# Kernel tuning notes

Measured on AMD Instinct MI355X. Metric: run time of the kernel, lower is better.

Reference implementation:

```python
import jax, jax.numpy as jnp
import numpy as np

TOP_K = 8  # top_k experts per token


def setup_inputs() -> dict:
    key = jax.random.key(0)
    k1, k2 = jax.random.split(key)
    T, H, E = 16384, 2048, 64
    hidden_states = jax.random.normal(k1, (T, H), dtype=jnp.float32)
    # nn.Linear(hidden_dim, num_experts, bias=False) weight: [E, H]
    gate_w = jax.random.normal(k2, (E, H), dtype=jnp.float32) * (1.0 / np.sqrt(H))
    expert_bias = jnp.zeros((E,), dtype=jnp.float32)  # aux_loss_free bias, init zeros
    return {"hidden_states": hidden_states, "gate_w": gate_w, "expert_bias": expert_bias}


def reference(hidden_states, gate_w, expert_bias):
    # logits: [T, E]
    logits = hidden_states @ gate_w.T
    scores = jax.nn.softmax(logits, axis=-1)  # score_func == 'softmax'
    # aux_loss_free: bias added only for expert selection, not to the probs
    selection_scores = scores + expert_bias[None, :]
    _, topk_indices = jax.lax.top_k(selection_scores, TOP_K)  # [T, K]
    probs = jnp.take_along_axis(scores, topk_indices, axis=-1)  # gather original scores
    probs = probs / (probs.sum(axis=-1, keepdims=True) + 1e-9)  # renormalize (softmax path)
    T, E = scores.shape
    routing_map = jnp.zeros((T, E), dtype=bool).at[jnp.arange(T)[:, None], topk_indices].set(True)
    aux_loss = jnp.zeros((), dtype=scores.dtype)  # load_balance == 'aux_loss_free' -> 0
    return probs, topk_indices, routing_map, aux_loss
```

## Files before the change

kernel.cpp:

```cpp
#include <hip/hip_runtime.h>
#include <math.h>

#define TT 16384
#define HH 2048
#define EE 64
#define KK 8

#define TB 16
#define HC 64
#define NCH (HH / HC)
#define KSPLIT 4
#define CPS (NCH / KSPLIT)
#define TOPC 10
#define MARGIN_REL 8e-5f

#define IDX_OFF ((size_t)TT * KK)
#define MAP_OFF ((size_t)2 * TT * KK)
#define AUX_OFF ((size_t)2 * TT * KK + (size_t)TT * EE)

#define WSPLANE 131072
#define PBUF_B   524288
#define NFLAG_B  17301504
#define LIST_B   17301536
#define RECI_B   17367072
#define RECF_B   18022432
#define NTILE (TT / TB)

typedef short bf16x8 __attribute__((ext_vector_type(8)));
typedef float f32x4  __attribute__((ext_vector_type(4)));

__device__ __forceinline__ unsigned short f2bf(float x) {
    unsigned int u = __float_as_uint(x);
    u += 0x7FFFu + ((u >> 16) & 1u);
    return (unsigned short)(u >> 16);
}
__device__ __forceinline__ float bf2f(unsigned short b) {
    return __uint_as_float(((unsigned int)b) << 16);
}
__device__ __forceinline__ void cvt4(const float4 v, ushort4* hi, ushort4* lo) {
    unsigned short h0 = f2bf(v.x), h1 = f2bf(v.y),
                   h2 = f2bf(v.z), h3 = f2bf(v.w);
    *hi = make_ushort4(h0, h1, h2, h3);
    *lo = make_ushort4(f2bf(v.x - bf2f(h0)), f2bf(v.y - bf2f(h1)),
                       f2bf(v.z - bf2f(h2)), f2bf(v.w - bf2f(h3)));
}

__global__ __launch_bounds__(256)
void prep_kernel(const float* __restrict__ gw, unsigned short* __restrict__ ws,
                 unsigned int* __restrict__ nflag)
{
    if (blockIdx.x == 0 && threadIdx.x == 0) *nflag = 0u;
    const int gid = blockIdx.x * 256 + threadIdx.x;
    const int e  = gid >> 9;
    const int k  = (gid & 511) * 4;
    float4 v = *(const float4*)(gw + (size_t)e * HH + k);
    ushort4 hi, lo;
    cvt4(v, &hi, &lo);
    const int off = (k >> 5) * 2048 + ((k >> 3) & 3) * 512 + e * 8 + (k & 7);
    *(ushort4*)(ws + off)           = hi;
    *(ushort4*)(ws + WSPLANE + off) = lo;
}

#define CHUNKA(C, HV)                                                          \
  do {                                                                         \
    const unsigned short* bp_ = bBase + (size_t)(2 * (C)) * 2048;              \
    bf16x8 Bh0 = *(const bf16x8*)(bp_);                                        \
    bf16x8 Bl0 = *(const bf16x8*)(bp_ + WSPLANE);                              \
    bf16x8 Bh1 = *(const bf16x8*)(bp_ + 2048);                                 \
    bf16x8 Bl1 = *(const bf16x8*)(bp_ + 2048 + WSPLANE);                       \
    unsigned char* buf_ = smem + ((C) & 1) * 4096;                             \
    ushort4 hi_, lo_;                                                          \
    cvt4(HV, &hi_, &lo_);                                                      \
    *(ushort4*)(buf_ + hOff)        = hi_;                                     \
    *(ushort4*)(buf_ + 2048 + hOff) = lo_;                                     \
    __syncthreads();                                                           \
    if ((C) + 2 < climit) HV = *(const float4*)(hgp + ((C) + 2) * HC);         \
    bf16x8 Ah0 = *(const bf16x8*)(buf_ + aOff0);                               \
    bf16x8 Al0 = *(const bf16x8*)(buf_ + 2048 + aOff0);                        \
    bf16x8 Ah1 = *(const bf16x8*)(buf_ + aOff1);                               \
    bf16x8 Al1 = *(const bf16x8*)(buf_ + 2048 + aOff1);                        \
    acc = __builtin_amdgcn_mfma_f32_16x16x32_bf16(Ah0, Bl0, acc, 0, 0, 0);     \
    acc = __builtin_amdgcn_mfma_f32_16x16x32_bf16(Al0, Bh0, acc, 0, 0, 0);     \
    acc = __builtin_amdgcn_mfma_f32_16x16x32_bf16(Ah0, Bh0, acc, 0, 0, 0);     \
    acc = __builtin_amdgcn_mfma_f32_16x16x32_bf16(Ah1, Bl1, acc, 0, 0, 0);     \
    acc = __builtin_amdgcn_mfma_f32_16x16x32_bf16(Al1, Bh1, acc, 0, 0, 0);     \
    acc = __builtin_amdgcn_mfma_f32_16x16x32_bf16(Ah1, Bh1, acc, 0, 0, 0);     \
  } while (0)

__global__ __launch_bounds__(256, 8)
void gemm_partial(const float* __restrict__ hidden,
                  const unsigned short* __restrict__ wsbuf,
                  float* __restrict__ pbuf)
{
    __shared__ __align__(16) unsigned char smem[8192];

    const int tid  = threadIdx.x;
    const int bid  = blockIdx.x;
    const int tile = bid >> 2;
    const int ks   = bid & 3;
    const int tok0 = tile * TB;
    const int c0   = ks * CPS;
    const int climit = c0 + CPS;

    const int hr  = tid >> 4;
    const int hc4 = tid & 15;
    const float* hgp = hidden + (size_t)(tok0 + hr) * HH + hc4 * 4;
    const int hOff = hr * 128 + ((hc4 * 8) ^ ((hr & 7) << 4));

    const int lane = tid & 63;
    const int e0   = (tid >> 6) * 16;
    const int rx   = lane & 15;
    const int kq   = lane >> 4;
    const int aOff0 = rx * 128 + ((kq * 16) ^ ((rx & 7) << 4));
    const int aOff1 = aOff0 ^ 64;
    const unsigned short* bBase = wsbuf + kq * 512 + (e0 + rx) * 8;

    f32x4 acc = {0.f, 0.f, 0.f, 0.f};

    float4 hvA = *(const float4*)(hgp + c0 * HC);
    float4 hvB = *(const float4*)(hgp + (c0 + 1) * HC);

    for (int c = c0; c < climit; c += 2) {
        CHUNKA(c, hvA);
        CHUNKA(c + 1, hvB);
    }

    *(f32x4*)(pbuf + (size_t)bid * 1024 + tid * 4) = acc;
}

__global__ __launch_bounds__(256, 4)
void reduce_epilogue(const float* __restrict__ pbuf,
                     const float* __restrict__ bias,
                     unsigned int* __restrict__ nflag,
                     unsigned int* __restrict__ list,
                     int* __restrict__ recI,
                     float* __restrict__ recF,
                     float* __restrict__ out)
{
    __shared__ __align__(16) float lg[16 * 68 + 8];

    const int tid  = threadIdx.x;
    const int tile = blockIdx.x;
    const int tok0 = tile * TB;

    f32x4 a0 = *(const f32x4*)(pbuf + (size_t)(tile * 4 + 0) * 1024 + tid * 4);
    f32x4 a1 = *(const f32x4*)(pbuf + (size_t)(tile * 4 + 1) * 1024 + tid * 4);
    f32x4 a2 = *(const f32x4*)(pbuf + (size_t)(tile * 4 + 2) * 1024 + tid * 4);
    f32x4 a3 = *(const f32x4*)(pbuf + (size_t)(tile * 4 + 3) * 1024 + tid * 4);
    f32x4 acc = (a0 + a1) + (a2 + a3);

    const int lane = tid & 63;
    const int e0   = (tid >> 6) * 16;
    const int rx   = lane & 15;
    const int kq   = lane >> 4;

    #pragma unroll
    for (int r = 0; r < 4; ++r)
        lg[(4 * kq + r) * 68 + e0 + rx] = acc[r];
    __syncthreads();

    const int t   = tid >> 4;
    const int q   = tid & 15;
    const int tok = tok0 + t;

    float lv[4];
    #pragma unroll
    for (int i = 0; i < 4; ++i) lv[i] = lg[t * 68 + q + 16 * i];

    float mx = lv[0];
    #pragma unroll
    for (int i = 1; i < 4; ++i) mx = fmaxf(mx, lv[i]);
    #pragma unroll
    for (int sh = 1; sh < 16; sh <<= 1) mx = fmaxf(mx, __shfl_xor(mx, sh, 64));

    float ex[4], psum = 0.0f;
    #pragma unroll
    for (int i = 0; i < 4; ++i) { ex[i] = expf(lv[i] - mx); psum += ex[i]; }
    #pragma unroll
    for (int sh = 1; sh < 16; sh <<= 1) psum += __shfl_xor(psum, sh, 64);
    const float inv = 1.0f / psum;

    float pr[4], selv[4];
    #pragma unroll
    for (int i = 0; i < 4; ++i) {
        pr[i]   = ex[i] * inv;
        selv[i] = pr[i] + bias[q + 16 * i];
    }

    float ws_[TOPC], wp[TOPC];
    int   wi[TOPC];
    #pragma unroll
    for (int k = 0; k < TOPC; ++k) {
        float bs = selv[0], bp = pr[0];
        int bi = q;
        #pragma unroll
        for (int i = 1; i < 4; ++i)
            if (selv[i] > bs) { bs = selv[i]; bp = pr[i]; bi = q + 16 * i; }
        #pragma unroll
        for (int sh = 1; sh < 16; sh <<= 1) {
            float os = __shfl_xor(bs, sh, 64);
            float op = __shfl_xor(bp, sh, 64);
            int   ob = __shfl_xor(bi, sh, 64);
            if (os > bs || (os == bs && ob < bi)) { bs = os; bp = op; bi = ob; }
        }
        ws_[k] = bs; wp[k] = bp; wi[k] = bi;
        #pragma unroll
        for (int i = 0; i < 4; ++i)
            if (q + 16 * i == bi) selv[i] = -INFINITY;
    }

    bool flag = false;
    #pragma unroll
    for (int k = 0; k < 8; ++k)
        flag = flag || (ws_[k] - ws_[k + 1] <
                        (ws_[k] + ws_[k + 1]) * MARGIN_REL + 1e-12f);

    {
        int   mywi = wi[0];
        float mywp = wp[0];
        #pragma unroll
        for (int k = 1; k < TOPC; ++k)
            if (q == k) { mywi = wi[k]; mywp = wp[k]; }
        if (flag && q < TOPC) {
            recI[(size_t)tok * 10 + q] = mywi;
            recF[(size_t)tok * 12 + q] = mywp;
        }
        if (flag && q == 0) {
            recF[(size_t)tok * 12 + 10] = mx;
            recF[(size_t)tok * 12 + 11] = inv;
            unsigned int o = atomicAdd(nflag, 1u);
            list[o] = (unsigned int)tok;
        }
    }

    int oi = wi[0];
    float opf = wp[0];
    #pragma unroll
    for (int k = 1; k < 8; ++k)
        if (q == k) { oi = wi[k]; opf = wp[k]; }

    float ps = 0.0f;
    #pragma unroll
    for (int k = 0; k < 8; ++k) ps += wp[k];
    const float rinv = 1.0f / (ps + 1e-9f);

    if (q < KK) {
        out[(size_t)tok * KK + q]           = opf * rinv;
        out[IDX_OFF + (size_t)tok * KK + q] = (float)oi;
    }

    unsigned long long mk = 0ull;
    #pragma unroll
    for (int k = 0; k < 8; ++k) mk |= (1ull << wi[k]);

    {
        float4 a;
        a.x = ((mk >> (4 * q + 0)) & 1ull) ? 1.0f : 0.0f;
        a.y = ((mk >> (4 * q + 1)) & 1ull) ? 1.0f : 0.0f;
        a.z = ((mk >> (4 * q + 2)) & 1ull) ? 1.0f : 0.0f;
        a.w = ((mk >> (4 * q + 3)) & 1ull) ? 1.0f : 0.0f;
        *(float4*)(out + MAP_OFF + (size_t)tok * EE + 4 * q) = a;
    }

    if (tile == 0 && tid == 0) out[AUX_OFF] = 0.0f;
}

__global__ __launch_bounds__(256, 4)
void fixup_kernel(const float* __restrict__ hidden,
                  const float* __restrict__ gate_w,
                  const float* __restrict__ bias,
                  const unsigned int* __restrict__ nflag,
                  const unsigned int* __restrict__ list,
                  const int* __restrict__ recI,
                  const float* __restrict__ recF,
                  float* __restrict__ out)
{
    __shared__ double redL[4][12];

    const int tid  = threadIdx.x;
    const int wv   = tid >> 6;
    const int lane = tid & 63;
    const unsigned int nf = *nflag;

    for (unsigned int i = blockIdx.x; i < nf; i += gridDim.x) {
        const int tok = (int)list[i];

        int   wk[TOPC];
        #pragma unroll
        for (int k = 0; k < TOPC; ++k) wk[k] = recI[(size_t)tok * 10 + k];
        const float mx  = recF[(size_t)tok * 12 + 10];
        const float inv = recF[(size_t)tok * 12 + 11];

        const float* hp = hidden + (size_t)tok * HH + tid * 8;
        float4 ha = *(const float4*)(hp);
        float4 hb = *(const float4*)(hp + 4);
        double h0 = ha.x, h1 = ha.y, h2 = ha.z, h3 = ha.w;
        double h4 = hb.x, h5 = hb.y, h6 = hb.z, h7 = hb.w;

        double l64[TOPC];
        #pragma unroll
        for (int k = 0; k < TOPC; ++k) {
            const float* wpt = gate_w + (size_t)wk[k] * HH + tid * 8;
            float4 wa = *(const float4*)(wpt);
            float4 wb = *(const float4*)(wpt + 4);
            double s = 0.0;
            s = fma(h0, (double)wa.x, s); s = fma(h1, (double)wa.y, s);
            s = fma(h2, (double)wa.z, s); s = fma(h3, (double)wa.w, s);
            s = fma(h4, (double)wb.x, s); s = fma(h5, (double)wb.y, s);
            s = fma(h6, (double)wb.z, s); s = fma(h7, (double)wb.w, s);
            l64[k] = s;
        }
        #pragma unroll
        for (int k = 0; k < TOPC; ++k)
            #pragma unroll
            for (int sh = 1; sh < 64; sh <<= 1)
                l64[k] += __shfl_xor(l64[k], sh, 64);
        if (lane == 0)
            #pragma unroll
            for (int k = 0; k < TOPC; ++k) redL[wv][k] = l64[k];
        __syncthreads();

        if (tid == 0) {
            double s64[TOPC];
            int    wi2[TOPC];
            float  wp2[TOPC];
            #pragma unroll
            for (int k = 0; k < TOPC; ++k) {
                double lk = redL[0][k] + redL[1][k] + redL[2][k] + redL[3][k];
                s64[k] = exp(lk - (double)mx) * (double)inv +
                         (double)bias[wk[k]];
                wi2[k] = wk[k];
                wp2[k] = recF[(size_t)tok * 12 + k];
            }
            #pragma unroll
            for (int a = 0; a < 8; ++a) {
                #pragma unroll
                for (int b = a + 1; b < TOPC; ++b) {
                    bool sw = (s64[b] > s64[a]) ||
                              (s64[b] == s64[a] && wi2[b] < wi2[a]);
                    if (sw) {
                        double td = s64[a]; s64[a] = s64[b]; s64[b] = td;
                        int    ti = wi2[a]; wi2[a] = wi2[b]; wi2[b] = ti;
                        float  tp = wp2[a]; wp2[a] = wp2[b]; wp2[b] = tp;
                    }
                }
            }
            float ps = 0.0f;
            #pragma unroll
            for (int k = 0; k < 8; ++k) ps += wp2[k];
            const float rinv = 1.0f / (ps + 1e-9f);
            unsigned long long mk = 0ull;
            #pragma unroll
            for (int k = 0; k < 8; ++k) {
                out[(size_t)tok * KK + k]           = wp2[k] * rinv;
                out[IDX_OFF + (size_t)tok * KK + k] = (float)wi2[k];
                mk |= (1ull << wi2[k]);
            }
            for (int e = 0; e < EE; ++e)
                out[MAP_OFF + (size_t)tok * EE + e] =
                    ((mk >> e) & 1ull) ? 1.0f : 0.0f;
        }
        __syncthreads();
    }
}

extern "C" void kernel_launch(void* const* d_in, const int* in_sizes, int n_in,
                              void* d_out, int out_size, void* d_ws, size_t ws_size,
                              hipStream_t stream) {
    const float* hidden = (const float*)d_in[0];
    const float* gate_w = (const float*)d_in[1];
    const float* bias   = (const float*)d_in[2];
    float* out = (float*)d_out;

    char* wsb = (char*)d_ws;
    unsigned short* wplanes = (unsigned short*)wsb;
    float*        pbuf  = (float*)(wsb + PBUF_B);
    unsigned int* nflag = (unsigned int*)(wsb + NFLAG_B);
    unsigned int* list  = (unsigned int*)(wsb + LIST_B);
    int*          recI  = (int*)(wsb + RECI_B);
    float*        recF  = (float*)(wsb + RECF_B);

    prep_kernel<<<128, 256, 0, stream>>>(gate_w, wplanes, nflag);
    gemm_partial<<<NTILE * KSPLIT, 256, 0, stream>>>(hidden, wplanes, pbuf);
    reduce_epilogue<<<NTILE, 256, 0, stream>>>(pbuf, bias, nflag, list,
                                               recI, recF, out);
    fixup_kernel<<<256, 256, 0, stream>>>(hidden, gate_w, bias, nflag, list,
                                          recI, recF, out);
}
```

Before: 65.23 us.

## Fuse split-K GEMM and reduce epilogue with per-wave K split in one block

```diff
diff --git a/kernel.cpp b/kernel.cpp
--- a/kernel.cpp
+++ b/kernel.cpp
@@ -19,11 +19,10 @@
 #define AUX_OFF ((size_t)2 * TT * KK + (size_t)TT * EE)
 
 #define WSPLANE 131072
-#define PBUF_B   524288
-#define NFLAG_B  17301504
-#define LIST_B   17301536
-#define RECI_B   17367072
-#define RECF_B   18022432
+#define NFLAG_B  524288
+#define LIST_B   524320
+#define RECI_B   589856
+#define RECF_B   1245216
 #define NTILE (TT / TB)
 
 typedef short bf16x8 __attribute__((ext_vector_type(8)));
@@ -61,102 +60,113 @@
     *(ushort4*)(ws + WSPLANE + off) = lo;
 }
 
-#define CHUNKA(C, HV)                                                          \
+#define MM(ET, AH, AL, BP, UOFF)                                               \
+  {                                                                            \
+    bf16x8 Bh = *(const bf16x8*)((BP) + (UOFF) + (ET) * 128);                  \
+    bf16x8 Bl = *(const bf16x8*)((BP) + (UOFF) + (ET) * 128 + WSPLANE);        \
+    acc##ET = __builtin_amdgcn_mfma_f32_16x16x32_bf16(AH, Bl, acc##ET, 0,0,0); \
+    acc##ET = __builtin_amdgcn_mfma_f32_16x16x32_bf16(AL, Bh, acc##ET, 0,0,0); \
+    acc##ET = __builtin_amdgcn_mfma_f32_16x16x32_bf16(AH, Bh, acc##ET, 0,0,0); \
+  }
+
+#define CHUNKW(C, A0, A1, A2, A3)                                              \
   do {                                                                         \
-    const unsigned short* bp_ = bBase + (size_t)(2 * (C)) * 2048;              \
-    bf16x8 Bh0 = *(const bf16x8*)(bp_);                                        \
-    bf16x8 Bl0 = *(const bf16x8*)(bp_ + WSPLANE);                              \
-    bf16x8 Bh1 = *(const bf16x8*)(bp_ + 2048);                                 \
-    bf16x8 Bl1 = *(const bf16x8*)(bp_ + 2048 + WSPLANE);                       \
-    unsigned char* buf_ = smem + ((C) & 1) * 4096;                             \
+    unsigned char* buf_ = wbuf + ((C) & 1) * 4096;                             \
     ushort4 hi_, lo_;                                                          \
-    cvt4(HV, &hi_, &lo_);                                                      \
-    *(ushort4*)(buf_ + hOff)        = hi_;                                     \
-    *(ushort4*)(buf_ + 2048 + hOff) = lo_;                                     \
-    __syncthreads();                                                           \
-    if ((C) + 2 < climit) HV = *(const float4*)(hgp + ((C) + 2) * HC);         \
-    bf16x8 Ah0 = *(const bf16x8*)(buf_ + aOff0);                               \
-    bf16x8 Al0 = *(const bf16x8*)(buf_ + 2048 + aOff0);                        \
-    bf16x8 Ah1 = *(const bf16x8*)(buf_ + aOff1);                               \
-    bf16x8 Al1 = *(const bf16x8*)(buf_ + 2048 + aOff1);                        \
-    acc = __builtin_amdgcn_mfma_f32_16x16x32_bf16(Ah0, Bl0, acc, 0, 0, 0);     \
-    acc = __builtin_amdgcn_mfma_f32_16x16x32_bf16(Al0, Bh0, acc, 0, 0, 0);     \
-    acc = __builtin_amdgcn_mfma_f32_16x16x32_bf16(Ah0, Bh0, acc, 0, 0, 0);     \
-    acc = __builtin_amdgcn_mfma_f32_16x16x32_bf16(Ah1, Bl1, acc, 0, 0, 0);     \
-    acc = __builtin_amdgcn_mfma_f32_16x16x32_bf16(Al1, Bh1, acc, 0, 0, 0);     \
-    acc = __builtin_amdgcn_mfma_f32_16x16x32_bf16(Ah1, Bh1, acc, 0, 0, 0);     \
+    cvt4(A0, &hi_, &lo_);                                                      \
+    *(ushort4*)(buf_ + wOff0) = hi_; *(ushort4*)(buf_ + 2048 + wOff0) = lo_;   \
+    cvt4(A1, &hi_, &lo_);                                                      \
+    *(ushort4*)(buf_ + wOff1) = hi_; *(ushort4*)(buf_ + 2048 + wOff1) = lo_;   \
+    cvt4(A2, &hi_, &lo_);                                                      \
+    *(ushort4*)(buf_ + wOff2) = hi_; *(ushort4*)(buf_ + 2048 + wOff2) = lo_;   \
+    cvt4(A3, &hi_, &lo_);                                                      \
+    *(ushort4*)(buf_ + wOff3) = hi_; *(ushort4*)(buf_ + 2048 + wOff3) = lo_;   \
+    if ((C) + 2 < CPS) {                                                       \
+      const float* hp_ = hgp + (c0 + (C) + 2) * HC;                            \
+      A0 = *(const float4*)(hp_);      A1 = *(const float4*)(hp_ + 16);        \
+      A2 = *(const float4*)(hp_ + 32); A3 = *(const float4*)(hp_ + 48);        \
+    }                                                                          \
+    const unsigned short* bp_ = bBase + (size_t)(2 * (c0 + (C))) * 2048;       \
+    {                                                                          \
+      bf16x8 Ah = *(const bf16x8*)(buf_ + aOff0);                              \
+      bf16x8 Al = *(const bf16x8*)(buf_ + 2048 + aOff0);                       \
+      MM(0, Ah, Al, bp_, 0) MM(1, Ah, Al, bp_, 0)                              \
+      MM(2, Ah, Al, bp_, 0) MM(3, Ah, Al, bp_, 0)                              \
+    }                                                                          \
+    {                                                                          \
+      bf16x8 Ah = *(const bf16x8*)(buf_ + aOff1);                              \
+      bf16x8 Al = *(const bf16x8*)(buf_ + 2048 + aOff1);                       \
+      MM(0, Ah, Al, bp_, 2048) MM(1, Ah, Al, bp_, 2048)                        \
+      MM(2, Ah, Al, bp_, 2048) MM(3, Ah, Al, bp_, 2048)                        \
+    }                                                                          \
   } while (0)
 
-__global__ __launch_bounds__(256, 8)
-void gemm_partial(const float* __restrict__ hidden,
-                  const unsigned short* __restrict__ wsbuf,
-                  float* __restrict__ pbuf)
+__global__ __launch_bounds__(256, 4)
+void fused_gemm(const float* __restrict__ hidden,
+                const float* __restrict__ bias,
+                const unsigned short* __restrict__ wsbuf,
+                unsigned int* __restrict__ nflag,
+                unsigned int* __restrict__ list,
+                int* __restrict__ recI,
+                float* __restrict__ recF,
+                float* __restrict__ out)
 {
-    __shared__ __align__(16) unsigned char smem[8192];
+    __shared__ __align__(16) unsigned char smem[32768];
 
     const int tid  = threadIdx.x;
-    const int bid  = blockIdx.x;
-    const int tile = bid >> 2;
-    const int ks   = bid & 3;
+    const int w    = tid >> 6;
+    const int lane = tid & 63;
+    const int tile = blockIdx.x;
     const int tok0 = tile * TB;
-    const int c0   = ks * CPS;
-    const int climit = c0 + CPS;
-
-    const int hr  = tid >> 4;
-    const int hc4 = tid & 15;
-    const float* hgp = hidden + (size_t)(tok0 + hr) * HH + hc4 * 4;
-    const int hOff = hr * 128 + ((hc4 * 8) ^ ((hr & 7) << 4));
-
-    const int lane = tid & 63;
-    const int e0   = (tid >> 6) * 16;
-    const int rx   = lane & 15;
-    const int kq   = lane >> 4;
+    const int c0   = w * CPS;
+
+    const int hr = lane >> 2;
+    const int q4 = lane & 3;
+    const float* hgp = hidden + (size_t)(tok0 + hr) * HH + q4 * 4;
+    unsigned char* wbuf = smem + w * 8192;
+    const int key = (hr & 7) << 4;
+    const int wOff0 = hr * 128 + (((q4 + 0)  * 8) ^ key);
+    const int wOff1 = hr * 128 + (((q4 + 4)  * 8) ^ key);
+    const int wOff2 = hr * 128 + (((q4 + 8)  * 8) ^ key);
+    const int wOff3 = hr * 128 + (((q4 + 12) * 8) ^ key);
+
+    const int rx = lane & 15;
+    const int kq = lane >> 4;
     const int aOff0 = rx * 128 + ((kq * 16) ^ ((rx & 7) << 4));
     const int aOff1 = aOff0 ^ 64;
-    const unsigned short* bBase = wsbuf + kq * 512 + (e0 + rx) * 8;
-
-    f32x4 acc = {0.f, 0.f, 0.f, 0.f};
-
-    float4 hvA = *(const float4*)(hgp + c0 * HC);
-    float4 hvB = *(const float4*)(hgp + (c0 + 1) * HC);
-
-    for (int c = c0; c < climit; c += 2) {
-        CHUNKA(c, hvA);
-        CHUNKA(c + 1, hvB);
-    }
-
-    *(f32x4*)(pbuf + (size_t)bid * 1024 + tid * 4) = acc;
-}
-
-__global__ __launch_bounds__(256, 4)
-void reduce_epilogue(const float* __restrict__ pbuf,
-                     const float* __restrict__ bias,
-                     unsigned int* __restrict__ nflag,
-                     unsigned int* __restrict__ list,
-                     int* __restrict__ recI,
-                     float* __restrict__ recF,
-                     float* __restrict__ out)
-{
-    __shared__ __align__(16) float lg[16 * 68 + 8];
-
-    const int tid  = threadIdx.x;
-    const int tile = blockIdx.x;
-    const int tok0 = tile * TB;
-
-    f32x4 a0 = *(const f32x4*)(pbuf + (size_t)(tile * 4 + 0) * 1024 + tid * 4);
-    f32x4 a1 = *(const f32x4*)(pbuf + (size_t)(tile * 4 + 1) * 1024 + tid * 4);
-    f32x4 a2 = *(const f32x4*)(pbuf + (size_t)(tile * 4 + 2) * 1024 + tid * 4);
-    f32x4 a3 = *(const f32x4*)(pbuf + (size_t)(tile * 4 + 3) * 1024 + tid * 4);
-    f32x4 acc = (a0 + a1) + (a2 + a3);
-
-    const int lane = tid & 63;
-    const int e0   = (tid >> 6) * 16;
-    const int rx   = lane & 15;
-    const int kq   = lane >> 4;
-
-    #pragma unroll
-    for (int r = 0; r < 4; ++r)
-        lg[(4 * kq + r) * 68 + e0 + rx] = acc[r];
+    const unsigned short* bBase = wsbuf + kq * 512 + rx * 8;
+
+    f32x4 acc0 = {0.f,0.f,0.f,0.f}, acc1 = {0.f,0.f,0.f,0.f};
+    f32x4 acc2 = {0.f,0.f,0.f,0.f}, acc3 = {0.f,0.f,0.f,0.f};
+
+    float4 a0, a1, a2, a3, b0, b1, b2, b3;
+    {
+        const float* hp = hgp + c0 * HC;
+        a0 = *(const float4*)(hp);      a1 = *(const float4*)(hp + 16);
+        a2 = *(const float4*)(hp + 32); a3 = *(const float4*)(hp + 48);
+        const float* hq = hgp + (c0 + 1) * HC;
+        b0 = *(const float4*)(hq);      b1 = *(const float4*)(hq + 16);
+        b2 = *(const float4*)(hq + 32); b3 = *(const float4*)(hq + 48);
+    }
+
+    for (int c = 0; c < CPS; c += 2) {
+        CHUNKW(c,     a0, a1, a2, a3);
+        CHUNKW(c + 1, b0, b1, b2, b3);
+    }
+
+    __syncthreads();
+    float* red = (float*)smem;
+    {
+        float* rw = red + w * 1088;
+        #pragma unroll
+        for (int r = 0; r < 4; ++r) {
+            const int row = (4 * kq + r) * 68 + rx;
+            rw[row +  0] = acc0[r];
+            rw[row + 16] = acc1[r];
+            rw[row + 32] = acc2[r];
+            rw[row + 48] = acc3[r];
+        }
+    }
     __syncthreads();
 
     const int t   = tid >> 4;
@@ -165,7 +175,10 @@
 
     float lv[4];
     #pragma unroll
-    for (int i = 0; i < 4; ++i) lv[i] = lg[t * 68 + q + 16 * i];
+    for (int i = 0; i < 4; ++i) {
+        const int o = t * 68 + q + 16 * i;
+        lv[i] = (red[o] + red[1088 + o]) + (red[2176 + o] + red[3264 + o]);
+    }
 
     float mx = lv[0];
     #pragma unroll
@@ -374,16 +387,14 @@
 
     char* wsb = (char*)d_ws;
     unsigned short* wplanes = (unsigned short*)wsb;
-    float*        pbuf  = (float*)(wsb + PBUF_B);
     unsigned int* nflag = (unsigned int*)(wsb + NFLAG_B);
     unsigned int* list  = (unsigned int*)(wsb + LIST_B);
     int*          recI  = (int*)(wsb + RECI_B);
     float*        recF  = (float*)(wsb + RECF_B);
 
     prep_kernel<<<128, 256, 0, stream>>>(gate_w, wplanes, nflag);
-    gemm_partial<<<NTILE * KSPLIT, 256, 0, stream>>>(hidden, wplanes, pbuf);
-    reduce_epilogue<<<NTILE, 256, 0, stream>>>(pbuf, bias, nflag, list,
-                                               recI, recF, out);
+    fused_gemm<<<NTILE, 256, 0, stream>>>(hidden, bias, wplanes, nflag, list,
+                                          recI, recF, out);
     fixup_kernel<<<256, 256, 0, stream>>>(hidden, gate_w, bias, nflag, list,
                                           recI, recF, out);
 }
```

After: 62.10 us. 1.05x faster.
